# Optimization experiments

Hardware: AMD Instinct MI355X
Metric: run time of the kernel (lower is better)

Reference implementation:

```python
import jax, jax.numpy as jnp
import numpy as np

H = 8
DH = 64  # attention_head_size
HID = 512
NEG = -90000000000.0

def _lin(x, w, b):
    return x @ w + b

def _tfs(x):  # [N, HID] -> [H, N, DH]
    n = x.shape[0]
    return x.reshape(n, H, DH).transpose(1, 0, 2)

def _cross(q, ck, v, cv, mask, dw, db):
    # q: [H,N,DH], ck/cv: [H,M,DH], v: [H,N,DH], mask: [N,M]
    s = jnp.einsum('hnd,hmd->hnm', q, ck)
    s = s * mask[None, :, :] / jnp.sqrt(jnp.asarray(DH, s.dtype))
    s = jnp.where(s == 0.0, NEG, s)  # faithful zero->-inf hack
    p = jax.nn.softmax(s, axis=-1)
    ctx = v + jnp.einsum('hnm,hmd->hnd', p, cv)  # residual add of raw value
    n = ctx.shape[1]
    ctx = ctx.transpose(1, 0, 2).reshape(n, H * DH)
    return _lin(ctx, dw, db)

def setup_inputs() -> dict:
    key = jax.random.key(0)
    ks = jax.random.split(key, 24)
    N1, N2, D1 = 4096, 4096, 300
    d = {}
    d['h_head'] = jax.random.normal(ks[0], (N1, D1), jnp.float32)
    d['h_tail'] = jax.random.normal(ks[1], (N2, HID), jnp.float32)
    d['batch_head'] = jnp.sort(jax.random.randint(ks[2], (N1,), 0, 64))
    d['batch_tail'] = jnp.sort(jax.random.randint(ks[3], (N2,), 0, 64))
    def w(k, i, o):
        return jax.random.normal(k, (i, o), jnp.float32) / np.sqrt(i)
    d['map_w'] = w(ks[4], D1, HID); d['map_b'] = jnp.zeros((HID,), jnp.float32)
    names = ['q1', 'k1', 'v1', 'q2', 'k2', 'v2', 'd1', 'd2']
    for i, nm in enumerate(names):
        d[nm + '_w'] = w(ks[5 + i], HID, HID)
        d[nm + '_b'] = jnp.zeros((HID,), jnp.float32)
    return d

def reference(h_head, h_tail, batch_head, batch_tail,
              map_w, map_b,
              q1_w, q1_b, k1_w, k1_b, v1_w, v1_b,
              q2_w, q2_b, k2_w, k2_b, v2_w, v2_b,
              d1_w, d1_b, d2_w, d2_b):
    hh = _lin(h_head, map_w, map_b)  # n_dim1 != n_dim2 -> map
    q_h = _tfs(_lin(hh, q1_w, q1_b))
    k_h = _tfs(_lin(hh, k1_w, k1_b))
    v_h = _tfs(_lin(hh, v1_w, v1_b))
    q_t = _tfs(_lin(h_tail, q2_w, q2_b))
    k_t = _tfs(_lin(h_tail, k2_w, k2_b))
    v_t = _tfs(_lin(h_tail, v2_w, v2_b))
    mask = (batch_head[:, None] == batch_tail[None, :]).astype(jnp.float32)
    out_head = _cross(q_h, k_t, v_h, v_t, mask, d1_w, d1_b)
    out_tail = _cross(q_t, k_h, v_t, v_h, mask.T, d2_w, d2_b)
    return (out_head, out_tail)
```

## Files before the change

### kernel.cpp

```cpp
#include <hip/hip_runtime.h>
#include <hip/hip_bf16.h>
#include <math.h>


typedef __bf16 bf16x8 __attribute__((ext_vector_type(8)));
typedef float  f32x4  __attribute__((ext_vector_type(4)));

#define HID 512
#define NTOK 4096
#define BM 64
#define BN 64
#define BK 32
#define LDSS 40

__global__ void compute_ranges(const int* __restrict__ bh,
                               const int* __restrict__ bt,
                               int n, int* __restrict__ out) {
    int t = threadIdx.x;
    if (t >= 128) return;
    int b = t & 63;
    const int* arr = (t < 64) ? bh : bt;
    int base = (t < 64) ? 0 : 128;
    int lo = 0, hi = n;
    while (lo < hi) { int mid = (lo + hi) >> 1; if (arr[mid] < b) lo = mid + 1; else hi = mid; }
    int start = lo;
    lo = 0; hi = n;
    while (lo < hi) { int mid = (lo + hi) >> 1; if (arr[mid] <= b) lo = mid + 1; else hi = mid; }
    out[base + b] = start;
    out[base + 64 + b] = lo;
}

struct TransJobs {
    const float* src[9];
    __bf16*      dst[9];
    int          K[9];
    int          ldT[9];
};

__global__ __launch_bounds__(256) void transpose_weights(TransJobs tj) {
    const int z = blockIdx.z;
    const float* src = tj.src[z];
    __bf16* dst = tj.dst[z];
    const int K = tj.K[z], ldT = tj.ldT[z];
    const int tk = blockIdx.y * 64;
    const int tn = blockIdx.x * 64;
    if (tk >= ldT) return;

    __shared__ __bf16 T[64][72];
    const int tid = threadIdx.x;
    const int r0 = tid >> 4;
    const int c0 = (tid & 15) * 4;
    #pragma unroll
    for (int i = 0; i < 4; ++i) {
        int k = tk + r0 + i * 16;
        float4 v = (k < K) ? *(const float4*)&src[(size_t)k * 512 + tn + c0]
                           : float4{0.f, 0.f, 0.f, 0.f};
        T[r0 + i * 16][c0 + 0] = (__bf16)v.x;
        T[r0 + i * 16][c0 + 1] = (__bf16)v.y;
        T[r0 + i * 16][c0 + 2] = (__bf16)v.z;
        T[r0 + i * 16][c0 + 3] = (__bf16)v.w;
    }
    __syncthreads();

    const int n  = tid >> 2;
    const int kk = (tid & 3) * 16;
    bf16x8 o0, o1;
    #pragma unroll
    for (int j = 0; j < 8; ++j) { o0[j] = T[kk + j][n]; o1[j] = T[kk + 8 + j][n]; }
    __bf16* dp = dst + (size_t)(tn + n) * ldT + tk + kk;
    *(bf16x8*)dp       = o0;
    *(bf16x8*)(dp + 8) = o1;
}

template <typename TA, typename TC>
__global__ __launch_bounds__(256) void gemm3(
    const TA* __restrict__ A0, const TA* __restrict__ A1, const TA* __restrict__ A2,
    int ldA,
    const __bf16* __restrict__ W0, const __bf16* __restrict__ W1, const __bf16* __restrict__ W2,
    const float* __restrict__ B0, const float* __restrict__ B1, const float* __restrict__ B2,
    TC* __restrict__ C0, TC* __restrict__ C1, TC* __restrict__ C2,
    int Kreal, int Kpad)
{
    __shared__ __align__(16) __bf16 As[BM][LDSS];
    __shared__ __align__(16) __bf16 Bs[BN][LDSS];

    const int z = blockIdx.z;
    const TA*     A    = z == 0 ? A0 : (z == 1 ? A1 : A2);
    const __bf16* WT   = z == 0 ? W0 : (z == 1 ? W1 : W2);
    const float*  bias = z == 0 ? B0 : (z == 1 ? B1 : B2);
    TC*           C    = z == 0 ? C0 : (z == 1 ? C1 : C2);

    const int tid  = threadIdx.x;
    const int wave = tid >> 6;
    const int lane = tid & 63;
    const int quad = lane >> 4;
    const int l16  = lane & 15;
    const int rowBase = blockIdx.y * BM;
    const int colBase = blockIdx.x * BN;

    const int s_row = tid >> 2;
    const int s_col = (tid & 3) * 8;

    f32x4 acc[4] = {};

    for (int kt = 0; kt < Kpad; kt += BK) {
        {
            const TA* Ap = A + (size_t)(rowBase + s_row) * ldA + kt + s_col;
            if constexpr (sizeof(TA) == 4) {
                if (kt + s_col + 8 <= Kreal) {
                    float4 f0 = *(const float4*)(Ap);
                    float4 f1 = *(const float4*)(Ap + 4);
                    bf16x8 v;
                    v[0]=(__bf16)f0.x; v[1]=(__bf16)f0.y; v[2]=(__bf16)f0.z; v[3]=(__bf16)f0.w;
                    v[4]=(__bf16)f1.x; v[5]=(__bf16)f1.y; v[6]=(__bf16)f1.z; v[7]=(__bf16)f1.w;
                    *(bf16x8*)&As[s_row][s_col] = v;
                } else {
                    #pragma unroll
                    for (int j = 0; j < 8; ++j) {
                        int k = kt + s_col + j;
                        As[s_row][s_col + j] = (k < Kreal) ? (__bf16)Ap[j] : (__bf16)0.f;
                    }
                }
            } else {
                *(bf16x8*)&As[s_row][s_col] = *(const bf16x8*)Ap;
            }
        }
        {
            const __bf16* Wp = WT + (size_t)(colBase + s_row) * Kpad + kt + s_col;
            *(bf16x8*)&Bs[s_row][s_col] = *(const bf16x8*)Wp;
        }
        __syncthreads();

        bf16x8 af = *(const bf16x8*)&As[wave * 16 + l16][quad * 8];
        #pragma unroll
        for (int c = 0; c < 4; ++c) {
            bf16x8 bf = *(const bf16x8*)&Bs[c * 16 + l16][quad * 8];
            acc[c] = __builtin_amdgcn_mfma_f32_16x16x32_bf16(af, bf, acc[c], 0, 0, 0);
        }
        __syncthreads();
    }

    #pragma unroll
    for (int c = 0; c < 4; ++c) {
        int col = colBase + c * 16 + l16;
        float bv = bias[col];
        #pragma unroll
        for (int r = 0; r < 4; ++r) {
            int row = rowBase + wave * 16 + quad * 4 + r;
            C[(size_t)row * HID + col] = (TC)(acc[c][r] + bv);
        }
    }
}

__global__ __launch_bounds__(256) void attn_mfma(
    const __bf16* __restrict__ Q0, const __bf16* __restrict__ K0,
    const __bf16* __restrict__ Vr0, const __bf16* __restrict__ Vc0,
    const __bf16* __restrict__ Q1, const __bf16* __restrict__ K1,
    const __bf16* __restrict__ Vr1, const __bf16* __restrict__ Vc1,
    const int* __restrict__ ranges,
    __bf16* __restrict__ O0, __bf16* __restrict__ O1,
    int Nq, int Nk)
{
    __shared__ __align__(16) __bf16 Qs[64][72];
    __shared__ __align__(16) __bf16 Ks[64][72];
    __shared__ __align__(16) __bf16 Vt[64][72];
    __shared__ __align__(16) __bf16 Ps[64][72];

    const int z = blockIdx.z;
    const __bf16* Q    = z ? Q1 : Q0;
    const __bf16* Kg   = z ? K1 : K0;
    const __bf16* Vres = z ? Vr1 : Vr0;
    const __bf16* Vctx = z ? Vc1 : Vc0;
    __bf16* Out        = z ? O1 : O0;
    const int* qstart  = z ? ranges + 128 : ranges;
    const int* qend    = z ? ranges + 192 : ranges + 64;
    const int* kstart  = z ? ranges       : ranges + 128;
    const int* kend    = z ? ranges + 64  : ranges + 192;

    const int h = blockIdx.x, b = blockIdx.y;
    const int qs = qstart[b], qe = qend[b];
    const int ts = kstart[b], te = kend[b];
    const int nq = qe - qs, nk = te - ts;
    if (nq <= 0) return;

    const int tid  = threadIdx.x;
    const int wave = tid >> 6;
    const int lane = tid & 63;
    const int quad = lane >> 4;
    const int l16  = lane & 15;
    const int srow = tid >> 2;
    const int scol = (tid & 3) * 16;

    if (nk <= 0) {
        float* meanv = (float*)Qs;
        if (tid < 64) {
            float s = 0.f;
            for (int m = 0; m < Nk; ++m)
                s += (float)Vctx[(size_t)m * HID + h * 64 + tid];
            meanv[tid] = s / (float)Nk;
        }
        __syncthreads();
        int d = tid & 63;
        for (int r = qs + (tid >> 6); r < qe; r += 4) {
            size_t off = (size_t)r * HID + h * 64 + d;
            Out[off] = (__bf16)((float)Vres[off] + meanv[d]);
        }
        return;
    }

    for (int qc = 0; qc < nq; qc += 64) {
        __syncthreads();
        {
            int qg = min(qs + qc + srow, Nq - 1);
            const __bf16* src = Q + (size_t)qg * HID + h * 64 + scol;
            *(bf16x8*)&Qs[srow][scol]     = *(const bf16x8*)src;
            *(bf16x8*)&Qs[srow][scol + 8] = *(const bf16x8*)(src + 8);
        }
        __syncthreads();
        bf16x8 aq0 = *(const bf16x8*)&Qs[wave * 16 + l16][quad * 8];
        bf16x8 aq1 = *(const bf16x8*)&Qs[wave * 16 + l16][32 + quad * 8];

        f32x4 O[4] = {};
        float Mx[4], L[4];
        #pragma unroll
        for (int r = 0; r < 4; ++r) { Mx[r] = -__builtin_inff(); L[r] = 0.f; }

        for (int kc = 0; kc < nk; kc += 64) {
            __syncthreads();
            {
                int kg = min(ts + kc + srow, Nk - 1);
                const __bf16* ksrc = Kg + (size_t)kg * HID + h * 64 + scol;
                *(bf16x8*)&Ks[srow][scol]     = *(const bf16x8*)ksrc;
                *(bf16x8*)&Ks[srow][scol + 8] = *(const bf16x8*)(ksrc + 8);
                const __bf16* vsrc = Vctx + (size_t)kg * HID + h * 64 + scol;
                bf16x8 v0 = *(const bf16x8*)vsrc;
                bf16x8 v1 = *(const bf16x8*)(vsrc + 8);
                #pragma unroll
                for (int j = 0; j < 8; ++j) {
                    Vt[scol + j][srow]     = v0[j];
                    Vt[scol + 8 + j][srow] = v1[j];
                }
            }
            __syncthreads();

            f32x4 S[4] = {};
            #pragma unroll
            for (int c = 0; c < 4; ++c) {
                bf16x8 bk0 = *(const bf16x8*)&Ks[c * 16 + l16][quad * 8];
                bf16x8 bk1 = *(const bf16x8*)&Ks[c * 16 + l16][32 + quad * 8];
                S[c] = __builtin_amdgcn_mfma_f32_16x16x32_bf16(aq0, bk0, S[c], 0, 0, 0);
                S[c] = __builtin_amdgcn_mfma_f32_16x16x32_bf16(aq1, bk1, S[c], 0, 0, 0);
            }

            #pragma unroll
            for (int c = 0; c < 4; ++c) {
                bool valid = (ts + kc + c * 16 + l16) < te;
                #pragma unroll
                for (int r = 0; r < 4; ++r)
                    S[c][r] = valid ? S[c][r] * 0.125f : -__builtin_inff();
            }

            float cm[4], ps[4], alpha[4];
            #pragma unroll
            for (int r = 0; r < 4; ++r) {
                float v = fmaxf(fmaxf(S[0][r], S[1][r]), fmaxf(S[2][r], S[3][r]));
                v = fmaxf(v, __shfl_xor(v, 1, 64));
                v = fmaxf(v, __shfl_xor(v, 2, 64));
                v = fmaxf(v, __shfl_xor(v, 4, 64));
                v = fmaxf(v, __shfl_xor(v, 8, 64));
                cm[r] = v;
            }
            #pragma unroll
            for (int r = 0; r < 4; ++r) {
                float nM = fmaxf(Mx[r], cm[r]);
                alpha[r] = __expf(Mx[r] - nM);
                Mx[r] = nM;
                ps[r] = 0.f;
            }
            #pragma unroll
            for (int c = 0; c < 4; ++c)
                #pragma unroll
                for (int r = 0; r < 4; ++r) {
                    float p = __expf(S[c][r] - Mx[r]);
                    S[c][r] = p;
                    ps[r] += p;
                }
            #pragma unroll
            for (int r = 0; r < 4; ++r) {
                float v = ps[r];
                v += __shfl_xor(v, 1, 64);
                v += __shfl_xor(v, 2, 64);
                v += __shfl_xor(v, 4, 64);
                v += __shfl_xor(v, 8, 64);
                L[r] = L[r] * alpha[r] + v;
            }
            #pragma unroll
            for (int c = 0; c < 4; ++c)
                #pragma unroll
                for (int r = 0; r < 4; ++r)
                    O[c][r] *= alpha[r];

            #pragma unroll
            for (int c = 0; c < 4; ++c)
                #pragma unroll
                for (int r = 0; r < 4; ++r)
                    Ps[wave * 16 + quad * 4 + r][c * 16 + l16] = (__bf16)S[c][r];
            __syncthreads();

            bf16x8 ap0 = *(const bf16x8*)&Ps[wave * 16 + l16][quad * 8];
            bf16x8 ap1 = *(const bf16x8*)&Ps[wave * 16 + l16][32 + quad * 8];
            #pragma unroll
            for (int c = 0; c < 4; ++c) {
                bf16x8 bv0 = *(const bf16x8*)&Vt[c * 16 + l16][quad * 8];
                bf16x8 bv1 = *(const bf16x8*)&Vt[c * 16 + l16][32 + quad * 8];
                O[c] = __builtin_amdgcn_mfma_f32_16x16x32_bf16(ap0, bv0, O[c], 0, 0, 0);
                O[c] = __builtin_amdgcn_mfma_f32_16x16x32_bf16(ap1, bv1, O[c], 0, 0, 0);
            }
        }

        #pragma unroll
        for (int c = 0; c < 4; ++c) {
            int d = h * 64 + c * 16 + l16;
            #pragma unroll
            for (int r = 0; r < 4; ++r) {
                int qrow = qs + qc + wave * 16 + quad * 4 + r;
                if (qrow < qe) {
                    size_t off = (size_t)qrow * HID + d;
                    Out[off] = (__bf16)((float)Vres[off] + O[c][r] / L[r]);
                }
            }
        }
    }
}

extern "C" void kernel_launch(void* const* d_in, const int* in_sizes, int n_in,
                              void* d_out, int out_size, void* d_ws, size_t ws_size,
                              hipStream_t stream) {
    (void)in_sizes; (void)n_in; (void)out_size; (void)ws_size;

    const float* h_head = (const float*)d_in[0];
    const float* h_tail = (const float*)d_in[1];
    const int* batch_head = (const int*)d_in[2];
    const int* batch_tail = (const int*)d_in[3];
    const float* map_w = (const float*)d_in[4];
    const float* map_b = (const float*)d_in[5];
    const float* q1_w = (const float*)d_in[6];
    const float* q1_b = (const float*)d_in[7];
    const float* k1_w = (const float*)d_in[8];
    const float* k1_b = (const float*)d_in[9];
    const float* v1_w = (const float*)d_in[10];
    const float* v1_b = (const float*)d_in[11];
    const float* q2_w = (const float*)d_in[12];
    const float* q2_b = (const float*)d_in[13];
    const float* k2_w = (const float*)d_in[14];
    const float* k2_b = (const float*)d_in[15];
    const float* v2_w = (const float*)d_in[16];
    const float* v2_b = (const float*)d_in[17];
    const float* d1_w = (const float*)d_in[18];
    const float* d1_b = (const float*)d_in[19];
    const float* d2_w = (const float*)d_in[20];
    const float* d2_b = (const float*)d_in[21];

    float* out = (float*)d_out;

    const size_t SZ = (size_t)NTOK * HID;
    char* ws = (char*)d_ws;
    int* ranges = (int*)ws;
    __bf16* hh   = (__bf16*)(ws + 1024);
    __bf16* qh   = hh  + SZ;
    __bf16* kh   = qh  + SZ;
    __bf16* vh   = kh  + SZ;
    __bf16* qt   = vh  + SZ;
    __bf16* kt   = qt  + SZ;
    __bf16* vt   = kt  + SZ;
    __bf16* ctxh = vt  + SZ;
    __bf16* ctxt = ctxh + SZ;
    __bf16* mapT = ctxt + SZ;
    __bf16* q1T  = mapT + 512 * 320;
    __bf16* k1T  = q1T + 512 * 512;
    __bf16* v1T  = k1T + 512 * 512;
    __bf16* q2T  = v1T + 512 * 512;
    __bf16* k2T  = q2T + 512 * 512;
    __bf16* v2T  = k2T + 512 * 512;
    __bf16* d1T  = v2T + 512 * 512;
    __bf16* d2T  = d1T + 512 * 512;

    compute_ranges<<<dim3(1), dim3(128), 0, stream>>>(batch_head, batch_tail, NTOK, ranges);

    TransJobs tj;
    tj.src[0] = map_w; tj.dst[0] = mapT; tj.K[0] = 300; tj.ldT[0] = 320;
    const float* wsrc[8] = {q1_w, k1_w, v1_w, q2_w, k2_w, v2_w, d1_w, d2_w};
    __bf16* wdst[8] = {q1T, k1T, v1T, q2T, k2T, v2T, d1T, d2T};
    for (int i = 0; i < 8; ++i) {
        tj.src[i + 1] = wsrc[i]; tj.dst[i + 1] = wdst[i];
        tj.K[i + 1] = 512; tj.ldT[i + 1] = 512;
    }
    transpose_weights<<<dim3(8, 8, 9), dim3(256), 0, stream>>>(tj);

    dim3 gblk(256);
    gemm3<float, __bf16><<<dim3(8, 64, 1), gblk, 0, stream>>>(
        h_head, h_head, h_head, 300,
        mapT, mapT, mapT, map_b, map_b, map_b,
        hh, hh, hh, 300, 320);
    gemm3<__bf16, __bf16><<<dim3(8, 64, 3), gblk, 0, stream>>>(
        hh, hh, hh, 512,
        q1T, k1T, v1T, q1_b, k1_b, v1_b,
        qh, kh, vh, 512, 512);
    gemm3<float, __bf16><<<dim3(8, 64, 3), gblk, 0, stream>>>(
        h_tail, h_tail, h_tail, 512,
        q2T, k2T, v2T, q2_b, k2_b, v2_b,
        qt, kt, vt, 512, 512);

    attn_mfma<<<dim3(8, 64, 2), dim3(256), 0, stream>>>(
        qh, kt, vh, vt,
        qt, kh, vt, vh,
        ranges, ctxh, ctxt, NTOK, NTOK);

    gemm3<__bf16, float><<<dim3(8, 64, 2), gblk, 0, stream>>>(
        ctxh, ctxt, ctxt, 512,
        d1T, d2T, d2T, d1_b, d2_b, d2_b,
        out, out + SZ, out + SZ, 512, 512);
}
```

Before: 207.4 us.

## Replace 64x64 GEMMs with 128x128 tiles using direct global-to-LDS loads

The fp32 inputs are converted to padded bf16 in a new prep kernel, which also computes the batch ranges. All projection GEMMs then run through a 128x128-tile kernel in which each wave computes a 4x4 grid of MFMA tiles, with operands staged through global_load_lds. The map projection is batched together with the tail QKV projections, so there are fewer launches and more operand reuse per tile. The cost is an extra pass over the inputs, larger per-block register and LDS footprint, and fewer blocks per launch.

```diff
diff --git a/kernel.cpp b/kernel.cpp
--- a/kernel.cpp
+++ b/kernel.cpp
@@ -8,26 +8,62 @@
 
 #define HID 512
 #define NTOK 4096
-#define BM 64
-#define BN 64
-#define BK 32
-#define LDSS 40
-
-__global__ void compute_ranges(const int* __restrict__ bh,
-                               const int* __restrict__ bt,
-                               int n, int* __restrict__ out) {
-    int t = threadIdx.x;
-    if (t >= 128) return;
-    int b = t & 63;
-    const int* arr = (t < 64) ? bh : bt;
-    int base = (t < 64) ? 0 : 128;
-    int lo = 0, hi = n;
-    while (lo < hi) { int mid = (lo + hi) >> 1; if (arr[mid] < b) lo = mid + 1; else hi = mid; }
-    int start = lo;
-    lo = 0; hi = n;
-    while (lo < hi) { int mid = (lo + hi) >> 1; if (arr[mid] <= b) lo = mid + 1; else hi = mid; }
-    out[base + b] = start;
-    out[base + 64 + b] = lo;
+
+#define AS1(p) ((const __attribute__((address_space(1))) void*)(p))
+#define AS3(p) ((__attribute__((address_space(3))) void*)(p))
+
+__global__ __launch_bounds__(256) void prep_inputs(
+    const float* __restrict__ h_head, const float* __restrict__ h_tail,
+    const int* __restrict__ bh, const int* __restrict__ bt,
+    __bf16* __restrict__ hh_bf, __bf16* __restrict__ ht_bf,
+    int* __restrict__ ranges)
+{
+    const int q = blockIdx.x, z = blockIdx.z, tid = threadIdx.x;
+
+    if (z == 0) {
+        if (q == 0 && tid < 128) {
+            int b = tid & 63;
+            const int* arr = (tid < 64) ? bh : bt;
+            int base = (tid < 64) ? 0 : 128;
+            int lo = 0, hi = NTOK;
+            while (lo < hi) { int mid = (lo + hi) >> 1; if (arr[mid] < b) lo = mid + 1; else hi = mid; }
+            int start = lo;
+            lo = 0; hi = NTOK;
+            while (lo < hi) { int mid = (lo + hi) >> 1; if (arr[mid] <= b) lo = mid + 1; else hi = mid; }
+            ranges[base + b] = start;
+            ranges[base + 64 + b] = lo;
+        }
+        for (int idx = tid; idx < 8 * 40; idx += 256) {
+            int r   = q * 8 + idx / 40;
+            int col = (idx % 40) * 8;
+            bf16x8 v;
+            if (col + 8 <= 300) {
+                float4 f0 = *(const float4*)&h_head[(size_t)r * 300 + col];
+                float4 f1 = *(const float4*)&h_head[(size_t)r * 300 + col + 4];
+                v[0]=(__bf16)f0.x; v[1]=(__bf16)f0.y; v[2]=(__bf16)f0.z; v[3]=(__bf16)f0.w;
+                v[4]=(__bf16)f1.x; v[5]=(__bf16)f1.y; v[6]=(__bf16)f1.z; v[7]=(__bf16)f1.w;
+            } else if (col < 300) {
+                float4 f0 = *(const float4*)&h_head[(size_t)r * 300 + col];
+                v[0]=(__bf16)f0.x; v[1]=(__bf16)f0.y; v[2]=(__bf16)f0.z; v[3]=(__bf16)f0.w;
+                v[4]=(__bf16)0.f; v[5]=(__bf16)0.f; v[6]=(__bf16)0.f; v[7]=(__bf16)0.f;
+            } else {
+                #pragma unroll
+                for (int j = 0; j < 8; ++j) v[j] = (__bf16)0.f;
+            }
+            *(bf16x8*)&hh_bf[(size_t)r * 320 + col] = v;
+        }
+    } else {
+        for (int idx = tid; idx < 8 * 64; idx += 256) {
+            int r   = q * 8 + (idx >> 6);
+            int col = (idx & 63) * 8;
+            float4 f0 = *(const float4*)&h_tail[(size_t)r * 512 + col];
+            float4 f1 = *(const float4*)&h_tail[(size_t)r * 512 + col + 4];
+            bf16x8 v;
+            v[0]=(__bf16)f0.x; v[1]=(__bf16)f0.y; v[2]=(__bf16)f0.z; v[3]=(__bf16)f0.w;
+            v[4]=(__bf16)f1.x; v[5]=(__bf16)f1.y; v[6]=(__bf16)f1.z; v[7]=(__bf16)f1.w;
+            *(bf16x8*)&ht_bf[(size_t)r * 512 + col] = v;
+        }
+    }
 }
 
 struct TransJobs {
@@ -72,82 +108,81 @@
     *(bf16x8*)(dp + 8) = o1;
 }
 
-template <typename TA, typename TC>
-__global__ __launch_bounds__(256) void gemm3(
-    const TA* __restrict__ A0, const TA* __restrict__ A1, const TA* __restrict__ A2,
-    int ldA,
-    const __bf16* __restrict__ W0, const __bf16* __restrict__ W1, const __bf16* __restrict__ W2,
-    const float* __restrict__ B0, const float* __restrict__ B1, const float* __restrict__ B2,
-    TC* __restrict__ C0, TC* __restrict__ C1, TC* __restrict__ C2,
-    int Kreal, int Kpad)
-{
-    __shared__ __align__(16) __bf16 As[BM][LDSS];
-    __shared__ __align__(16) __bf16 Bs[BN][LDSS];
+struct GemmJobs {
+    const __bf16* A[4];
+    const __bf16* W[4];
+    const float*  bias[4];
+    void*         C[4];
+    int           Kp[4];
+};
+
+template <typename TC>
+__global__ __launch_bounds__(256) void gemm128(GemmJobs jobs) {
+    __shared__ __align__(16) __bf16 As[128 * 32];
+    __shared__ __align__(16) __bf16 Bs[128 * 32];
 
     const int z = blockIdx.z;
-    const TA*     A    = z == 0 ? A0 : (z == 1 ? A1 : A2);
-    const __bf16* WT   = z == 0 ? W0 : (z == 1 ? W1 : W2);
-    const float*  bias = z == 0 ? B0 : (z == 1 ? B1 : B2);
-    TC*           C    = z == 0 ? C0 : (z == 1 ? C1 : C2);
+    const __bf16* A    = jobs.A[z];
+    const __bf16* W    = jobs.W[z];
+    const float*  bias = jobs.bias[z];
+    TC*           C    = (TC*)jobs.C[z];
+    const int     Kp   = jobs.Kp[z];
 
     const int tid  = threadIdx.x;
     const int wave = tid >> 6;
     const int lane = tid & 63;
     const int quad = lane >> 4;
     const int l16  = lane & 15;
-    const int rowBase = blockIdx.y * BM;
-    const int colBase = blockIdx.x * BN;
+    const int wy   = wave >> 1;
+    const int wx   = wave & 1;
+    const int rowBase = blockIdx.y * 128;
+    const int colBase = blockIdx.x * 128;
 
     const int s_row = tid >> 2;
-    const int s_col = (tid & 3) * 8;
-
-    f32x4 acc[4] = {};
-
-    for (int kt = 0; kt < Kpad; kt += BK) {
-        {
-            const TA* Ap = A + (size_t)(rowBase + s_row) * ldA + kt + s_col;
-            if constexpr (sizeof(TA) == 4) {
-                if (kt + s_col + 8 <= Kreal) {
-                    float4 f0 = *(const float4*)(Ap);
-                    float4 f1 = *(const float4*)(Ap + 4);
-                    bf16x8 v;
-                    v[0]=(__bf16)f0.x; v[1]=(__bf16)f0.y; v[2]=(__bf16)f0.z; v[3]=(__bf16)f0.w;
-                    v[4]=(__bf16)f1.x; v[5]=(__bf16)f1.y; v[6]=(__bf16)f1.z; v[7]=(__bf16)f1.w;
-                    *(bf16x8*)&As[s_row][s_col] = v;
-                } else {
-                    #pragma unroll
-                    for (int j = 0; j < 8; ++j) {
-                        int k = kt + s_col + j;
-                        As[s_row][s_col + j] = (k < Kreal) ? (__bf16)Ap[j] : (__bf16)0.f;
-                    }
-                }
-            } else {
-                *(bf16x8*)&As[s_row][s_col] = *(const bf16x8*)Ap;
-            }
-        }
-        {
-            const __bf16* Wp = WT + (size_t)(colBase + s_row) * Kpad + kt + s_col;
-            *(bf16x8*)&Bs[s_row][s_col] = *(const bf16x8*)Wp;
-        }
+    const int s_kc  = (tid & 3) * 8;
+
+    f32x4 acc[4][4] = {};
+
+    const __bf16* gA = A + (size_t)(rowBase + s_row) * Kp + s_kc;
+    const __bf16* gB = W + (size_t)(colBase + s_row) * Kp + s_kc;
+    __bf16* lA0 = &As[wave * 512];
+    __bf16* lA1 = &As[2048 + wave * 512];
+    __bf16* lB0 = &Bs[wave * 512];
+    __bf16* lB1 = &Bs[2048 + wave * 512];
+
+    for (int kt = 0; kt < Kp; kt += 32) {
+        __builtin_amdgcn_global_load_lds(AS1(gA + kt),            AS3(lA0), 16, 0, 0);
+        __builtin_amdgcn_global_load_lds(AS1(gA + kt + 64 * Kp),  AS3(lA1), 16, 0, 0);
+        __builtin_amdgcn_global_load_lds(AS1(gB + kt),            AS3(lB0), 16, 0, 0);
+        __builtin_amdgcn_global_load_lds(AS1(gB + kt + 64 * Kp),  AS3(lB1), 16, 0, 0);
         __syncthreads();
 
-        bf16x8 af = *(const bf16x8*)&As[wave * 16 + l16][quad * 8];
-        #pragma unroll
-        for (int c = 0; c < 4; ++c) {
-            bf16x8 bf = *(const bf16x8*)&Bs[c * 16 + l16][quad * 8];
-            acc[c] = __builtin_amdgcn_mfma_f32_16x16x32_bf16(af, bf, acc[c], 0, 0, 0);
-        }
+        bf16x8 ar[4], br[4];
+        #pragma unroll
+        for (int i = 0; i < 4; ++i)
+            ar[i] = *(const bf16x8*)&As[(wy * 64 + i * 16 + l16) * 32 + quad * 8];
+        #pragma unroll
+        for (int j = 0; j < 4; ++j)
+            br[j] = *(const bf16x8*)&Bs[(wx * 64 + j * 16 + l16) * 32 + quad * 8];
+        #pragma unroll
+        for (int i = 0; i < 4; ++i)
+            #pragma unroll
+            for (int j = 0; j < 4; ++j)
+                acc[i][j] = __builtin_amdgcn_mfma_f32_16x16x32_bf16(ar[i], br[j], acc[i][j], 0, 0, 0);
         __syncthreads();
     }
 
     #pragma unroll
-    for (int c = 0; c < 4; ++c) {
-        int col = colBase + c * 16 + l16;
+    for (int j = 0; j < 4; ++j) {
+        int col = colBase + wx * 64 + j * 16 + l16;
         float bv = bias[col];
         #pragma unroll
-        for (int r = 0; r < 4; ++r) {
-            int row = rowBase + wave * 16 + quad * 4 + r;
-            C[(size_t)row * HID + col] = (TC)(acc[c][r] + bv);
+        for (int i = 0; i < 4; ++i) {
+            #pragma unroll
+            for (int r = 0; r < 4; ++r) {
+                int row = rowBase + wy * 64 + i * 16 + quad * 4 + r;
+                C[(size_t)row * HID + col] = (TC)(acc[i][j][r] + bv);
+            }
         }
     }
 }
@@ -384,8 +419,11 @@
     __bf16* v2T  = k2T + 512 * 512;
     __bf16* d1T  = v2T + 512 * 512;
     __bf16* d2T  = d1T + 512 * 512;
-
-    compute_ranges<<<dim3(1), dim3(128), 0, stream>>>(batch_head, batch_tail, NTOK, ranges);
+    __bf16* hh_bf = d2T + 512 * 512;
+    __bf16* ht_bf = hh_bf + (size_t)NTOK * 320;
+
+    prep_inputs<<<dim3(512, 1, 2), dim3(256), 0, stream>>>(
+        h_head, h_tail, batch_head, batch_tail, hh_bf, ht_bf, ranges);
 
     TransJobs tj;
     tj.src[0] = map_w; tj.dst[0] = mapT; tj.K[0] = 300; tj.ldT[0] = 320;
@@ -397,27 +435,34 @@
     }
     transpose_weights<<<dim3(8, 8, 9), dim3(256), 0, stream>>>(tj);
 
-    dim3 gblk(256);
-    gemm3<float, __bf16><<<dim3(8, 64, 1), gblk, 0, stream>>>(
-        h_head, h_head, h_head, 300,
-        mapT, mapT, mapT, map_b, map_b, map_b,
-        hh, hh, hh, 300, 320);
-    gemm3<__bf16, __bf16><<<dim3(8, 64, 3), gblk, 0, stream>>>(
-        hh, hh, hh, 512,
-        q1T, k1T, v1T, q1_b, k1_b, v1_b,
-        qh, kh, vh, 512, 512);
-    gemm3<float, __bf16><<<dim3(8, 64, 3), gblk, 0, stream>>>(
-        h_tail, h_tail, h_tail, 512,
-        q2T, k2T, v2T, q2_b, k2_b, v2_b,
-        qt, kt, vt, 512, 512);
+    {
+        GemmJobs j;
+        j.A[0] = hh_bf; j.W[0] = mapT; j.bias[0] = map_b; j.C[0] = hh; j.Kp[0] = 320;
+        j.A[1] = ht_bf; j.W[1] = q2T; j.bias[1] = q2_b; j.C[1] = qt; j.Kp[1] = 512;
+        j.A[2] = ht_bf; j.W[2] = k2T; j.bias[2] = k2_b; j.C[2] = kt; j.Kp[2] = 512;
+        j.A[3] = ht_bf; j.W[3] = v2T; j.bias[3] = v2_b; j.C[3] = vt; j.Kp[3] = 512;
+        gemm128<__bf16><<<dim3(4, 32, 4), dim3(256), 0, stream>>>(j);
+    }
+    {
+        GemmJobs j;
+        j.A[0] = hh; j.W[0] = q1T; j.bias[0] = q1_b; j.C[0] = qh; j.Kp[0] = 512;
+        j.A[1] = hh; j.W[1] = k1T; j.bias[1] = k1_b; j.C[1] = kh; j.Kp[1] = 512;
+        j.A[2] = hh; j.W[2] = v1T; j.bias[2] = v1_b; j.C[2] = vh; j.Kp[2] = 512;
+        j.A[3] = hh; j.W[3] = v1T; j.bias[3] = v1_b; j.C[3] = vh; j.Kp[3] = 512;
+        gemm128<__bf16><<<dim3(4, 32, 3), dim3(256), 0, stream>>>(j);
+    }
 
     attn_mfma<<<dim3(8, 64, 2), dim3(256), 0, stream>>>(
         qh, kt, vh, vt,
         qt, kh, vt, vh,
         ranges, ctxh, ctxt, NTOK, NTOK);
 
-    gemm3<__bf16, float><<<dim3(8, 64, 2), gblk, 0, stream>>>(
-        ctxh, ctxt, ctxt, 512,
-        d1T, d2T, d2T, d1_b, d2_b, d2_b,
-        out, out + SZ, out + SZ, 512, 512);
+    {
+        GemmJobs j;
+        j.A[0] = ctxh; j.W[0] = d1T; j.bias[0] = d1_b; j.C[0] = out;      j.Kp[0] = 512;
+        j.A[1] = ctxt; j.W[1] = d2T; j.bias[1] = d2_b; j.C[1] = out + SZ; j.Kp[1] = 512;
+        j.A[2] = ctxt; j.W[2] = d2T; j.bias[2] = d2_b; j.C[2] = out + SZ; j.Kp[2] = 512;
+        j.A[3] = ctxt; j.W[3] = d2T; j.bias[3] = d2_b; j.C[3] = out + SZ; j.Kp[3] = 512;
+        gemm128<float><<<dim3(4, 32, 2), dim3(256), 0, stream>>>(j);
+    }
 }
```

After: 191.7 us. 1.08x faster.
